# Performance work log

Measured on AMD Instinct MI355X. Metric: run time of the kernel, lower is better.

## Reference

```python
import jax, jax.numpy as jnp
import numpy as np

N, M, D, H = 100000, 1600000, 128, 1
ITERS = 10          # props
ALPHA = 0.1
GAMMA = 1.0 - ALPHA # self.gamma = ones(1,H,C)*(1-alpha)
EPS = 1e-16


def _xavier(key, fan_in, fan_out):
    bound = float(np.sqrt(6.0 / (fan_in + fan_out)))
    return jax.random.uniform(key, (fan_in, fan_out), jnp.float32, -bound, bound)


def setup_inputs() -> dict:
    key = jax.random.key(0)
    k0, k1, k2, k3 = jax.random.split(key, 4)
    x = jax.random.normal(k0, (N, D), jnp.float32)
    e = jax.random.randint(k1, (2, M), 0, N, dtype=jnp.int64)
    lin_w = _xavier(k2, D, D)          # self.lin_w
    lin_b = jnp.zeros((1, H, D // H), jnp.float32)  # self.lin_b
    skip_w = _xavier(k3, D, D)         # self.skip_connections[0]
    ln_g = jnp.ones((D,), jnp.float32)  # LayerNorm weight
    ln_b = jnp.zeros((D,), jnp.float32) # LayerNorm bias
    return {"x": x, "e": e, "lin_w": lin_w, "lin_b": lin_b,
            "skip_w": skip_w, "ln_g": ln_g, "ln_b": ln_b}


def _ppr_power(e, w, x, gamma, iters):
    # PPR.ppr with power-iteration solver, tol=0, basis=None, T=False.
    n = x.shape[0]
    s = jax.lax.stop_gradient(jnp.max(jnp.abs(x)))  # x.detach().abs().max()
    xs = x / s

    def spmv(z):
        # scatter(w.unsqueeze(-1) * z[e[1]], e[0], dim=0, reduce='sum')
        src = w[..., None] * z[e[1]]                 # (m, H, C)
        return jax.ops.segment_sum(src, e[0], num_segments=n)

    def step(z, _):
        z = gamma * spmv(z) + (1.0 - gamma) * xs
        return z, None

    z, _ = jax.lax.scan(step, jnp.zeros_like(xs), None, length=iters)
    return z * s


def reference(x, e, lin_w, lin_b, skip_w, ln_g, ln_b):
    n, m = x.shape[0], e.shape[1]
    C = D // H
    v = (x @ lin_w).reshape(n, H, C)

    # weighted=False branch: w = zeros(m, H) -> attention logits are 0,
    # softmax over each source node's out-edges gives w_ij = 1/deg(i).
    deg = jax.ops.segment_sum(jnp.ones((m, H), x.dtype), e[0], num_segments=n)
    w = 1.0 / (deg + EPS)[e[0]]                      # (m, H)

    z = _ppr_power(e, w, v, GAMMA, ITERS)            # (n, H, C)

    # skip connection + bias + post LayerNorm
    z = z + (x @ skip_w).reshape(n, H, C)
    z = (z + lin_b).reshape(n, D)
    mu = jnp.mean(z, axis=-1, keepdims=True)
    var = jnp.mean((z - mu) ** 2, axis=-1, keepdims=True)
    out = (z - mu) * jax.lax.rsqrt(var + 1e-5) * ln_g + ln_b
    return out
```

## Files before the change

### kernel.cpp

```cpp
#include <hip/hip_runtime.h>
#include <hip/hip_bf16.h>

#define N_NODES 100000
#define M_EDGES 1600000
#define DIM 128

#define BUCKET_SHIFT 9
#define BUCKET_NODES 512
#define NB 196
#define CAP 10240
#define PA_BLOCKS 512
#define PA_CHUNK (M_EDGES / PA_BLOCKS)

typedef unsigned int uint32;
typedef unsigned short ushort;
typedef __attribute__((ext_vector_type(8))) short short8;
typedef __attribute__((ext_vector_type(4))) float f32x4;
typedef __attribute__((ext_vector_type(2))) float f32x2;

__device__ __forceinline__ uint32 pack_bf16_pair(float a, float b) {
    uint32 ua = __float_as_uint(a);
    uint32 ub = __float_as_uint(b);
    ua += 0x7fffu + ((ua >> 16) & 1u);
    ub += 0x7fffu + ((ub >> 16) & 1u);
    return (ua >> 16) | (ub & 0xffff0000u);
}
__device__ __forceinline__ ushort bf16_1(float f) {
    uint32 u = __float_as_uint(f);
    u += 0x7fffu + ((u >> 16) & 1u);
    return (ushort)(u >> 16);
}
__device__ __forceinline__ float2 unpack_bf16_pair(uint32 u) {
    float2 r;
    r.x = __uint_as_float(u << 16);
    r.y = __uint_as_float(u & 0xffff0000u);
    return r;
}

__device__ __forceinline__ uint32 pack2_fp8(float a, float b) {
    return (uint32)__builtin_amdgcn_cvt_pk_fp8_f32(a, b, 0, false);
}
__device__ __forceinline__ f32x2 unpack2_fp8(uint32 u) {
    return __builtin_amdgcn_cvt_pk_f32_fp8((int)u, false);
}

__global__ __launch_bounds__(256) void partA(const int* __restrict__ e0,
                                             const int* __restrict__ e1,
                                             int* __restrict__ g_cnt,
                                             uint32* __restrict__ pairs) {
    __shared__ int hist[NB];
    __shared__ int base[NB];
    const int tid = threadIdx.x;
    const int beg = blockIdx.x * PA_CHUNK;
    const int end = beg + PA_CHUNK;
    for (int i = tid; i < NB; i += 256) hist[i] = 0;
    __syncthreads();
    #pragma unroll 4
    for (int i = beg + tid; i < end; i += 256)
        atomicAdd(&hist[e0[i] >> BUCKET_SHIFT], 1);
    __syncthreads();
    for (int i = tid; i < NB; i += 256) {
        base[i] = atomicAdd(&g_cnt[i], hist[i]);
        hist[i] = 0;
    }
    __syncthreads();
    #pragma unroll 4
    for (int i = beg + tid; i < end; i += 256) {
        const int d = e0[i];
        const int s = e1[i];
        const int b = d >> BUCKET_SHIFT;
        const int off = atomicAdd(&hist[b], 1);
        pairs[b * CAP + base[b] + off] =
            ((uint32)s << BUCKET_SHIFT) | (uint32)(d & (BUCKET_NODES - 1));
    }
}

__global__ __launch_bounds__(256) void bucket_scan(const int* __restrict__ g_cnt,
                                                   int* __restrict__ g_base,
                                                   int* __restrict__ row_ptr) {
    __shared__ int woff[4];
    const int tid  = threadIdx.x;
    const int lane = tid & 63;
    const int wid  = tid >> 6;
    const int val  = (tid < NB) ? g_cnt[tid] : 0;
    int incl = val;
    #pragma unroll
    for (int o = 1; o < 64; o <<= 1) {
        int t = __shfl_up(incl, o, 64);
        if (lane >= o) incl += t;
    }
    if (lane == 63) woff[wid] = incl;
    __syncthreads();
    if (tid == 0) {
        int a = woff[0], b = woff[1], c = woff[2];
        woff[0] = 0; woff[1] = a; woff[2] = a + b; woff[3] = a + b + c;
    }
    __syncthreads();
    if (tid < NB) g_base[tid] = woff[wid] + incl - val;
    if (tid == 0) row_ptr[N_NODES] = M_EDGES;
}

__global__ __launch_bounds__(256) void partB(const int* __restrict__ g_cnt,
                                             const int* __restrict__ g_base,
                                             const uint32* __restrict__ pairs,
                                             int* __restrict__ row_ptr,
                                             int* __restrict__ csr) {
    __shared__ int deg[BUCKET_NODES];
    __shared__ int off[BUCKET_NODES];
    __shared__ int woff[4];
    const int b     = blockIdx.x;
    const int cnt   = g_cnt[b];
    const int gbase = g_base[b];
    const int n0    = b << BUCKET_SHIFT;
    const int tid   = threadIdx.x;
    deg[tid] = 0;
    deg[tid + 256] = 0;
    __syncthreads();
    #pragma unroll 4
    for (int j = tid; j < cnt; j += 256)
        atomicAdd(&deg[pairs[b * CAP + j] & (BUCKET_NODES - 1)], 1);
    __syncthreads();
    const int lane = tid & 63;
    const int wid  = tid >> 6;
    const int d0 = deg[2 * tid];
    const int d1 = deg[2 * tid + 1];
    const int sum = d0 + d1;
    int incl = sum;
    #pragma unroll
    for (int o = 1; o < 64; o <<= 1) {
        int t = __shfl_up(incl, o, 64);
        if (lane >= o) incl += t;
    }
    if (lane == 63) woff[wid] = incl;
    __syncthreads();
    if (tid == 0) {
        int a = woff[0], bb = woff[1], c = woff[2];
        woff[0] = 0; woff[1] = a; woff[2] = a + bb; woff[3] = a + bb + c;
    }
    __syncthreads();
    const int excl = woff[wid] + incl - sum;
    off[2 * tid]     = excl;
    off[2 * tid + 1] = excl + d0;
    const int node0 = n0 + 2 * tid;
    if (node0 < N_NODES)     row_ptr[node0]     = gbase + excl;
    if (node0 + 1 < N_NODES) row_ptr[node0 + 1] = gbase + excl + d0;
    __syncthreads();
    #pragma unroll 4
    for (int j = tid; j < cnt; j += 256) {
        const uint32 code = pairs[b * CAP + j];
        const int l = code & (BUCKET_NODES - 1);
        const int p = atomicAdd(&off[l], 1);
        csr[gbase + p] = (int)(code >> BUCKET_SHIFT);
    }
}

__global__ __launch_bounds__(256) void convert_x(const float* __restrict__ x,
                                                 uint32* __restrict__ xb) {
    const int i = blockIdx.x * 256 + threadIdx.x;
    const float4 a = ((const float4*)x)[2 * i];
    const float4 b = ((const float4*)x)[2 * i + 1];
    uint4 o;
    o.x = pack_bf16_pair(a.x, a.y);
    o.y = pack_bf16_pair(a.z, a.w);
    o.z = pack_bf16_pair(b.x, b.y);
    o.w = pack_bf16_pair(b.z, b.w);
    ((uint4*)xb)[i] = o;
}

__global__ __launch_bounds__(256) void convert_w(const float* __restrict__ lin_w,
                                                 const float* __restrict__ skip_w,
                                                 ushort* __restrict__ wt) {
    const int t = blockIdx.x * 256 + threadIdx.x;
    const int c = t >> 7;
    const int k = t & 127;
    const float val = (c < DIM) ? lin_w[k * DIM + c] : skip_w[k * DIM + (c - DIM)];
    wt[t] = bf16_1(val);
}

__global__ __launch_bounds__(256) void gemm_mfma(const ushort* __restrict__ xb,
                                                 const ushort* __restrict__ wt,
                                                 ushort* __restrict__ vb,
                                                 ushort* __restrict__ skipb) {
    __shared__ short8 As[64 * 16];
    __shared__ short8 Bs[256 * 16];
    const int tid  = threadIdx.x;
    const int row0 = blockIdx.x * 64;

    #pragma unroll
    for (int it = 0; it < 4; ++it) {
        const int idx = it * 256 + tid;
        const int r = idx >> 4, c = idx & 15;
        short8 val = (short8)0;
        if (row0 + r < N_NODES)
            val = *(const short8*)&xb[(size_t)(row0 + r) * DIM + c * 8];
        As[r * 16 + (c ^ (r & 7))] = val;
    }
    #pragma unroll
    for (int it = 0; it < 16; ++it) {
        const int idx = it * 256 + tid;
        const int r = idx >> 4, c = idx & 15;
        Bs[r * 16 + (c ^ (r & 7))] = *(const short8*)&wt[(size_t)r * DIM + c * 8];
    }
    __syncthreads();

    const int lane = tid & 63;
    const int wid  = tid >> 6;
    const int n0   = wid * 64;
    const int lrow = lane & 15;
    const int lgrp = lane >> 4;

    f32x4 acc[4][4];
    #pragma unroll
    for (int m = 0; m < 4; ++m)
        #pragma unroll
        for (int n = 0; n < 4; ++n) acc[m][n] = (f32x4)0.f;

    #pragma unroll
    for (int kk = 0; kk < 4; ++kk) {
        const int ch = kk * 4 + lgrp;
        short8 a[4], b[4];
        #pragma unroll
        for (int m = 0; m < 4; ++m) {
            const int r = m * 16 + lrow;
            a[m] = As[r * 16 + (ch ^ (r & 7))];
        }
        #pragma unroll
        for (int n = 0; n < 4; ++n) {
            const int r = n0 + n * 16 + lrow;
            b[n] = Bs[r * 16 + (ch ^ (r & 7))];
        }
        #pragma unroll
        for (int m = 0; m < 4; ++m)
            #pragma unroll
            for (int n = 0; n < 4; ++n)
                acc[m][n] = __builtin_amdgcn_mfma_f32_16x16x32_bf16(a[m], b[n], acc[m][n], 0, 0, 0);
    }

    ushort* dst = (wid < 2) ? vb : skipb;
    const int cbase = (wid < 2) ? n0 : n0 - 128;
    #pragma unroll
    for (int m = 0; m < 4; ++m) {
        #pragma unroll
        for (int n = 0; n < 4; ++n) {
            #pragma unroll
            for (int r = 0; r < 4; ++r) {
                const int row = row0 + m * 16 + lgrp * 4 + r;
                if (row < N_NODES)
                    dst[(size_t)row * DIM + cbase + n * 16 + lrow] = bf16_1(acc[m][n][r]);
            }
        }
    }
}

__global__ __launch_bounds__(256) void ppr_init_fp8(const uint32* __restrict__ vb,
                                                    uint32* __restrict__ z) {
    const int i = blockIdx.x * 256 + threadIdx.x;
    const float2 a = unpack_bf16_pair(vb[2 * i]);
    const float2 b = unpack_bf16_pair(vb[2 * i + 1]);
    int p = __builtin_amdgcn_cvt_pk_fp8_f32(0.1f * a.x, 0.1f * a.y, 0, false);
    p = __builtin_amdgcn_cvt_pk_fp8_f32(0.1f * b.x, 0.1f * b.y, p, true);
    z[i] = (uint32)p;
}

__global__ __launch_bounds__(256) void spmv_fp8(const int* __restrict__ row_ptr,
                                                const int* __restrict__ csr,
                                                const ushort* __restrict__ zin,
                                                const uint32* __restrict__ vb,
                                                ushort* __restrict__ zout) {
    const int node = blockIdx.x * 4 + (threadIdx.x >> 6);
    if (node >= N_NODES) return;
    const int lane  = threadIdx.x & 63;
    const int start = row_ptr[node];
    const int end   = row_ptr[node + 1];
    float ax0 = 0.f, ay0 = 0.f, ax1 = 0.f, ay1 = 0.f;
    float ax2 = 0.f, ay2 = 0.f, ax3 = 0.f, ay3 = 0.f;
    int j = start;
    for (; j + 4 <= end; j += 4) {
        const int s0 = csr[j], s1 = csr[j + 1], s2 = csr[j + 2], s3 = csr[j + 3];
        const f32x2 t0 = unpack2_fp8(zin[(size_t)s0 * 64 + lane]);
        const f32x2 t1 = unpack2_fp8(zin[(size_t)s1 * 64 + lane]);
        const f32x2 t2 = unpack2_fp8(zin[(size_t)s2 * 64 + lane]);
        const f32x2 t3 = unpack2_fp8(zin[(size_t)s3 * 64 + lane]);
        ax0 += t0.x; ay0 += t0.y;
        ax1 += t1.x; ay1 += t1.y;
        ax2 += t2.x; ay2 += t2.y;
        ax3 += t3.x; ay3 += t3.y;
    }
    for (; j < end; ++j) {
        const f32x2 t0 = unpack2_fp8(zin[(size_t)csr[j] * 64 + lane]);
        ax0 += t0.x; ay0 += t0.y;
    }
    const float invd = 1.0f / ((float)(end - start) + 1e-16f);
    const float2 vv = unpack_bf16_pair(vb[(size_t)node * 64 + lane]);
    const float ox = 0.9f * ((ax0 + ax1) + (ax2 + ax3)) * invd + 0.1f * vv.x;
    const float oy = 0.9f * ((ay0 + ay1) + (ay2 + ay3)) * invd + 0.1f * vv.y;
    zout[(size_t)node * 64 + lane] = (ushort)pack2_fp8(ox, oy);
}

__global__ __launch_bounds__(256) void spmv_final_ln(const int* __restrict__ row_ptr,
                                                     const int* __restrict__ csr,
                                                     const ushort* __restrict__ zin,
                                                     const uint32* __restrict__ vb,
                                                     const uint32* __restrict__ skipb,
                                                     const float* __restrict__ lin_b,
                                                     const float* __restrict__ ln_g,
                                                     const float* __restrict__ ln_b,
                                                     float* __restrict__ out) {
    const int node = blockIdx.x * 4 + (threadIdx.x >> 6);
    if (node >= N_NODES) return;
    const int lane  = threadIdx.x & 63;
    const int start = row_ptr[node];
    const int end   = row_ptr[node + 1];
    float ax0 = 0.f, ay0 = 0.f, ax1 = 0.f, ay1 = 0.f;
    float ax2 = 0.f, ay2 = 0.f, ax3 = 0.f, ay3 = 0.f;
    int j = start;
    for (; j + 4 <= end; j += 4) {
        const int s0 = csr[j], s1 = csr[j + 1], s2 = csr[j + 2], s3 = csr[j + 3];
        const f32x2 t0 = unpack2_fp8(zin[(size_t)s0 * 64 + lane]);
        const f32x2 t1 = unpack2_fp8(zin[(size_t)s1 * 64 + lane]);
        const f32x2 t2 = unpack2_fp8(zin[(size_t)s2 * 64 + lane]);
        const f32x2 t3 = unpack2_fp8(zin[(size_t)s3 * 64 + lane]);
        ax0 += t0.x; ay0 += t0.y;
        ax1 += t1.x; ay1 += t1.y;
        ax2 += t2.x; ay2 += t2.y;
        ax3 += t3.x; ay3 += t3.y;
    }
    for (; j < end; ++j) {
        const f32x2 t0 = unpack2_fp8(zin[(size_t)csr[j] * 64 + lane]);
        ax0 += t0.x; ay0 += t0.y;
    }
    const float invd = 1.0f / ((float)(end - start) + 1e-16f);
    const float2 vv = unpack_bf16_pair(vb[(size_t)node * 64 + lane]);
    const float2 sk = unpack_bf16_pair(skipb[(size_t)node * 64 + lane]);
    const float2 lb = *(const float2*)&lin_b[lane * 2];
    float tx = 0.9f * ((ax0 + ax1) + (ax2 + ax3)) * invd + 0.1f * vv.x + sk.x + lb.x;
    float ty = 0.9f * ((ay0 + ay1) + (ay2 + ay3)) * invd + 0.1f * vv.y + sk.y + lb.y;

    float s = tx + ty;
    float q = tx * tx + ty * ty;
    #pragma unroll
    for (int off = 32; off; off >>= 1) {
        s += __shfl_xor(s, off, 64);
        q += __shfl_xor(q, off, 64);
    }
    const float mu   = s * (1.0f / 128.0f);
    const float var  = q * (1.0f / 128.0f) - mu * mu;
    const float rstd = rsqrtf(var + 1e-5f);
    const float2 g = *(const float2*)&ln_g[lane * 2];
    const float2 b = *(const float2*)&ln_b[lane * 2];
    float2 o;
    o.x = (tx - mu) * rstd * g.x + b.x;
    o.y = (ty - mu) * rstd * g.y + b.y;
    *(float2*)&out[(size_t)node * DIM + lane * 2] = o;
}

extern "C" void kernel_launch(void* const* d_in, const int* in_sizes, int n_in,
                              void* d_out, int out_size, void* d_ws, size_t ws_size,
                              hipStream_t stream) {
    const float* x      = (const float*)d_in[0];
    const int*   e      = (const int*)d_in[1];
    const float* lin_w  = (const float*)d_in[2];
    const float* lin_b  = (const float*)d_in[3];
    const float* skip_w = (const float*)d_in[4];
    const float* ln_g   = (const float*)d_in[5];
    const float* ln_b   = (const float*)d_in[6];
    float* out = (float*)d_out;

    const int* e0 = e;
    const int* e1 = e + M_EDGES;

    char* ws = (char*)d_ws;
    const size_t hsz = (size_t)N_NODES * DIM * sizeof(ushort);
    const size_t qsz = (size_t)N_NODES * DIM;
    const size_t psz = (size_t)NB * CAP * sizeof(uint32);
    ushort* vb    = (ushort*)(ws);
    ushort* skipb = (ushort*)(ws + hsz);
    ushort* xb    = (ushort*)(ws + 2 * hsz);
    ushort* zA    = (ushort*)(ws + 3 * hsz);
    ushort* zB    = (ushort*)(ws + 3 * hsz + qsz);
    ushort* wt    = (ushort*)(ws + 3 * hsz + 2 * qsz);
    uint32* pairs = (uint32*)(ws + 3 * hsz + 2 * qsz + 65536);
    int* row_ptr  = (int*)(ws + 3 * hsz + 2 * qsz + 65536 + psz);
    int* g_cnt    = row_ptr + (N_NODES + 1);
    int* g_base   = g_cnt + NB;
    int* csr      = g_base + NB + 2;

    hipMemsetAsync(g_cnt, 0, NB * sizeof(int), stream);
    partA<<<PA_BLOCKS, 256, 0, stream>>>(e0, e1, g_cnt, pairs);
    bucket_scan<<<1, 256, 0, stream>>>(g_cnt, g_base, row_ptr);
    partB<<<NB, 256, 0, stream>>>(g_cnt, g_base, pairs, row_ptr, csr);

    convert_x<<<(N_NODES * DIM / 8) / 256, 256, 0, stream>>>(x, (uint32*)xb);
    convert_w<<<(2 * DIM * DIM) / 256, 256, 0, stream>>>(lin_w, skip_w, wt);
    gemm_mfma<<<(N_NODES + 63) / 64, 256, 0, stream>>>(xb, wt, vb, skipb);

    ppr_init_fp8<<<(N_NODES * DIM / 4) / 256, 256, 0, stream>>>((const uint32*)vb, (uint32*)zA);
    for (int it = 0; it < 8; ++it) {
        const ushort* zi = (it & 1) ? zB : zA;
        ushort*       zo = (it & 1) ? zA : zB;
        spmv_fp8<<<N_NODES / 4, 256, 0, stream>>>(row_ptr, csr, zi, (const uint32*)vb, zo);
    }
    spmv_final_ln<<<N_NODES / 4, 256, 0, stream>>>(row_ptr, csr, zA, (const uint32*)vb,
                                                   (const uint32*)skipb, lin_b, ln_g, ln_b, out);
}
```

Baseline: 802.2 us.

## Process two nodes per wavefront in SpMV and fuse x conversion into GEMM

SpMV kernels now assign a half-wavefront (32 lanes) per node, with each lane loading 4 fp8 values as one 32-bit word. This doubles nodes per block and halves the gather instructions per edge, improving memory-level parallelism for low-degree rows. The two halves loop up to the larger degree, with masked tail iterations, so imbalance between the paired nodes wastes some lanes. Separately, the fp32-to-bf16 conversion of x is folded into the GEMM tile load, removing the convert_x kernel and the bf16 copy of x in workspace.

```diff
diff --git a/kernel.cpp b/kernel.cpp
--- a/kernel.cpp
+++ b/kernel.cpp
@@ -37,11 +37,15 @@
     return r;
 }
 
-__device__ __forceinline__ uint32 pack2_fp8(float a, float b) {
-    return (uint32)__builtin_amdgcn_cvt_pk_fp8_f32(a, b, 0, false);
-}
-__device__ __forceinline__ f32x2 unpack2_fp8(uint32 u) {
-    return __builtin_amdgcn_cvt_pk_f32_fp8((int)u, false);
+__device__ __forceinline__ uint32 pack4_fp8(float a, float b, float c, float d) {
+    int p = __builtin_amdgcn_cvt_pk_fp8_f32(a, b, 0, false);
+    p = __builtin_amdgcn_cvt_pk_fp8_f32(c, d, p, true);
+    return (uint32)p;
+}
+__device__ __forceinline__ float4 unpack4_fp8(uint32 u) {
+    const f32x2 lo = __builtin_amdgcn_cvt_pk_f32_fp8((int)u, false);
+    const f32x2 hi = __builtin_amdgcn_cvt_pk_f32_fp8((int)u, true);
+    return make_float4(lo.x, lo.y, hi.x, hi.y);
 }
 
 __global__ __launch_bounds__(256) void partA(const int* __restrict__ e0,
@@ -154,19 +158,6 @@
     }
 }
 
-__global__ __launch_bounds__(256) void convert_x(const float* __restrict__ x,
-                                                 uint32* __restrict__ xb) {
-    const int i = blockIdx.x * 256 + threadIdx.x;
-    const float4 a = ((const float4*)x)[2 * i];
-    const float4 b = ((const float4*)x)[2 * i + 1];
-    uint4 o;
-    o.x = pack_bf16_pair(a.x, a.y);
-    o.y = pack_bf16_pair(a.z, a.w);
-    o.z = pack_bf16_pair(b.x, b.y);
-    o.w = pack_bf16_pair(b.z, b.w);
-    ((uint4*)xb)[i] = o;
-}
-
 __global__ __launch_bounds__(256) void convert_w(const float* __restrict__ lin_w,
                                                  const float* __restrict__ skip_w,
                                                  ushort* __restrict__ wt) {
@@ -177,12 +168,12 @@
     wt[t] = bf16_1(val);
 }
 
-__global__ __launch_bounds__(256) void gemm_mfma(const ushort* __restrict__ xb,
+__global__ __launch_bounds__(256) void gemm_mfma(const float* __restrict__ x,
                                                  const ushort* __restrict__ wt,
                                                  ushort* __restrict__ vb,
                                                  ushort* __restrict__ skipb) {
-    __shared__ short8 As[64 * 16];
-    __shared__ short8 Bs[256 * 16];
+    __shared__ uint4 As[64 * 16];
+    __shared__ uint4 Bs[256 * 16];
     const int tid  = threadIdx.x;
     const int row0 = blockIdx.x * 64;
 
@@ -190,16 +181,23 @@
     for (int it = 0; it < 4; ++it) {
         const int idx = it * 256 + tid;
         const int r = idx >> 4, c = idx & 15;
-        short8 val = (short8)0;
-        if (row0 + r < N_NODES)
-            val = *(const short8*)&xb[(size_t)(row0 + r) * DIM + c * 8];
-        As[r * 16 + (c ^ (r & 7))] = val;
+        const int row = row0 + r;
+        uint4 o = make_uint4(0, 0, 0, 0);
+        if (row < N_NODES) {
+            const float4 f0 = *(const float4*)&x[(size_t)row * DIM + c * 8];
+            const float4 f1 = *(const float4*)&x[(size_t)row * DIM + c * 8 + 4];
+            o.x = pack_bf16_pair(f0.x, f0.y);
+            o.y = pack_bf16_pair(f0.z, f0.w);
+            o.z = pack_bf16_pair(f1.x, f1.y);
+            o.w = pack_bf16_pair(f1.z, f1.w);
+        }
+        As[r * 16 + (c ^ (r & 7))] = o;
     }
     #pragma unroll
     for (int it = 0; it < 16; ++it) {
         const int idx = it * 256 + tid;
         const int r = idx >> 4, c = idx & 15;
-        Bs[r * 16 + (c ^ (r & 7))] = *(const short8*)&wt[(size_t)r * DIM + c * 8];
+        Bs[r * 16 + (c ^ (r & 7))] = *(const uint4*)&wt[(size_t)r * DIM + c * 8];
     }
     __syncthreads();
 
@@ -222,12 +220,12 @@
         #pragma unroll
         for (int m = 0; m < 4; ++m) {
             const int r = m * 16 + lrow;
-            a[m] = As[r * 16 + (ch ^ (r & 7))];
+            a[m] = *(const short8*)&As[r * 16 + (ch ^ (r & 7))];
         }
         #pragma unroll
         for (int n = 0; n < 4; ++n) {
             const int r = n0 + n * 16 + lrow;
-            b[n] = Bs[r * 16 + (ch ^ (r & 7))];
+            b[n] = *(const short8*)&Bs[r * 16 + (ch ^ (r & 7))];
         }
         #pragma unroll
         for (int m = 0; m < 4; ++m)
@@ -257,101 +255,139 @@
     const int i = blockIdx.x * 256 + threadIdx.x;
     const float2 a = unpack_bf16_pair(vb[2 * i]);
     const float2 b = unpack_bf16_pair(vb[2 * i + 1]);
-    int p = __builtin_amdgcn_cvt_pk_fp8_f32(0.1f * a.x, 0.1f * a.y, 0, false);
-    p = __builtin_amdgcn_cvt_pk_fp8_f32(0.1f * b.x, 0.1f * b.y, p, true);
-    z[i] = (uint32)p;
+    z[i] = pack4_fp8(0.1f * a.x, 0.1f * a.y, 0.1f * b.x, 0.1f * b.y);
 }
 
 __global__ __launch_bounds__(256) void spmv_fp8(const int* __restrict__ row_ptr,
                                                 const int* __restrict__ csr,
-                                                const ushort* __restrict__ zin,
+                                                const uint32* __restrict__ zin,
                                                 const uint32* __restrict__ vb,
-                                                ushort* __restrict__ zout) {
-    const int node = blockIdx.x * 4 + (threadIdx.x >> 6);
-    if (node >= N_NODES) return;
-    const int lane  = threadIdx.x & 63;
+                                                uint32* __restrict__ zout) {
+    const int node = blockIdx.x * 8 + (threadIdx.x >> 5);
+    const int l    = threadIdx.x & 31;
     const int start = row_ptr[node];
-    const int end   = row_ptr[node + 1];
-    float ax0 = 0.f, ay0 = 0.f, ax1 = 0.f, ay1 = 0.f;
-    float ax2 = 0.f, ay2 = 0.f, ax3 = 0.f, ay3 = 0.f;
-    int j = start;
-    for (; j + 4 <= end; j += 4) {
+    const int cnt   = row_ptr[node + 1] - start;
+    const int ocnt  = __shfl_xor(cnt, 32, 64);
+    const int mn = min(cnt, ocnt);
+    const int mx = max(cnt, ocnt);
+
+    float4 acc0 = make_float4(0.f, 0.f, 0.f, 0.f);
+    float4 acc1 = make_float4(0.f, 0.f, 0.f, 0.f);
+    int k = 0;
+    #pragma unroll 2
+    for (; k + 4 <= mn; k += 4) {
+        const int j = start + k;
         const int s0 = csr[j], s1 = csr[j + 1], s2 = csr[j + 2], s3 = csr[j + 3];
-        const f32x2 t0 = unpack2_fp8(zin[(size_t)s0 * 64 + lane]);
-        const f32x2 t1 = unpack2_fp8(zin[(size_t)s1 * 64 + lane]);
-        const f32x2 t2 = unpack2_fp8(zin[(size_t)s2 * 64 + lane]);
-        const f32x2 t3 = unpack2_fp8(zin[(size_t)s3 * 64 + lane]);
-        ax0 += t0.x; ay0 += t0.y;
-        ax1 += t1.x; ay1 += t1.y;
-        ax2 += t2.x; ay2 += t2.y;
-        ax3 += t3.x; ay3 += t3.y;
-    }
-    for (; j < end; ++j) {
-        const f32x2 t0 = unpack2_fp8(zin[(size_t)csr[j] * 64 + lane]);
-        ax0 += t0.x; ay0 += t0.y;
-    }
-    const float invd = 1.0f / ((float)(end - start) + 1e-16f);
-    const float2 vv = unpack_bf16_pair(vb[(size_t)node * 64 + lane]);
-    const float ox = 0.9f * ((ax0 + ax1) + (ax2 + ax3)) * invd + 0.1f * vv.x;
-    const float oy = 0.9f * ((ay0 + ay1) + (ay2 + ay3)) * invd + 0.1f * vv.y;
-    zout[(size_t)node * 64 + lane] = (ushort)pack2_fp8(ox, oy);
+        const uint32 w0 = zin[(s0 << 5) + l];
+        const uint32 w1 = zin[(s1 << 5) + l];
+        const uint32 w2 = zin[(s2 << 5) + l];
+        const uint32 w3 = zin[(s3 << 5) + l];
+        const float4 u0 = unpack4_fp8(w0);
+        const float4 u1 = unpack4_fp8(w1);
+        const float4 u2 = unpack4_fp8(w2);
+        const float4 u3 = unpack4_fp8(w3);
+        acc0.x += u0.x + u1.x; acc0.y += u0.y + u1.y;
+        acc0.z += u0.z + u1.z; acc0.w += u0.w + u1.w;
+        acc1.x += u2.x + u3.x; acc1.y += u2.y + u3.y;
+        acc1.z += u2.z + u3.z; acc1.w += u2.w + u3.w;
+    }
+    for (; k < mx; ++k) {
+        const bool valid = k < cnt;
+        const int j = valid ? start + k : 0;
+        const int s = csr[j];
+        const float4 u = unpack4_fp8(zin[(s << 5) + l]);
+        if (valid) {
+            acc0.x += u.x; acc0.y += u.y; acc0.z += u.z; acc0.w += u.w;
+        }
+    }
+    const float invd = 0.9f / ((float)cnt + 1e-16f);
+    const uint2 vv2 = *(const uint2*)&vb[(size_t)node * 64 + 2 * l];
+    const float2 va = unpack_bf16_pair(vv2.x);
+    const float2 vbp = unpack_bf16_pair(vv2.y);
+    const float ox = (acc0.x + acc1.x) * invd + 0.1f * va.x;
+    const float oy = (acc0.y + acc1.y) * invd + 0.1f * va.y;
+    const float oz = (acc0.z + acc1.z) * invd + 0.1f * vbp.x;
+    const float ow = (acc0.w + acc1.w) * invd + 0.1f * vbp.y;
+    zout[(node << 5) + l] = pack4_fp8(ox, oy, oz, ow);
 }
 
 __global__ __launch_bounds__(256) void spmv_final_ln(const int* __restrict__ row_ptr,
                                                      const int* __restrict__ csr,
-                                                     const ushort* __restrict__ zin,
+                                                     const uint32* __restrict__ zin,
                                                      const uint32* __restrict__ vb,
                                                      const uint32* __restrict__ skipb,
                                                      const float* __restrict__ lin_b,
                                                      const float* __restrict__ ln_g,
                                                      const float* __restrict__ ln_b,
                                                      float* __restrict__ out) {
-    const int node = blockIdx.x * 4 + (threadIdx.x >> 6);
-    if (node >= N_NODES) return;
-    const int lane  = threadIdx.x & 63;
+    const int node = blockIdx.x * 8 + (threadIdx.x >> 5);
+    const int l    = threadIdx.x & 31;
     const int start = row_ptr[node];
-    const int end   = row_ptr[node + 1];
-    float ax0 = 0.f, ay0 = 0.f, ax1 = 0.f, ay1 = 0.f;
-    float ax2 = 0.f, ay2 = 0.f, ax3 = 0.f, ay3 = 0.f;
-    int j = start;
-    for (; j + 4 <= end; j += 4) {
+    const int cnt   = row_ptr[node + 1] - start;
+    const int ocnt  = __shfl_xor(cnt, 32, 64);
+    const int mn = min(cnt, ocnt);
+    const int mx = max(cnt, ocnt);
+
+    float4 acc0 = make_float4(0.f, 0.f, 0.f, 0.f);
+    float4 acc1 = make_float4(0.f, 0.f, 0.f, 0.f);
+    int k = 0;
+    #pragma unroll 2
+    for (; k + 4 <= mn; k += 4) {
+        const int j = start + k;
         const int s0 = csr[j], s1 = csr[j + 1], s2 = csr[j + 2], s3 = csr[j + 3];
-        const f32x2 t0 = unpack2_fp8(zin[(size_t)s0 * 64 + lane]);
-        const f32x2 t1 = unpack2_fp8(zin[(size_t)s1 * 64 + lane]);
-        const f32x2 t2 = unpack2_fp8(zin[(size_t)s2 * 64 + lane]);
-        const f32x2 t3 = unpack2_fp8(zin[(size_t)s3 * 64 + lane]);
-        ax0 += t0.x; ay0 += t0.y;
-        ax1 += t1.x; ay1 += t1.y;
-        ax2 += t2.x; ay2 += t2.y;
-        ax3 += t3.x; ay3 += t3.y;
-    }
-    for (; j < end; ++j) {
-        const f32x2 t0 = unpack2_fp8(zin[(size_t)csr[j] * 64 + lane]);
-        ax0 += t0.x; ay0 += t0.y;
-    }
-    const float invd = 1.0f / ((float)(end - start) + 1e-16f);
-    const float2 vv = unpack_bf16_pair(vb[(size_t)node * 64 + lane]);
-    const float2 sk = unpack_bf16_pair(skipb[(size_t)node * 64 + lane]);
-    const float2 lb = *(const float2*)&lin_b[lane * 2];
-    float tx = 0.9f * ((ax0 + ax1) + (ax2 + ax3)) * invd + 0.1f * vv.x + sk.x + lb.x;
-    float ty = 0.9f * ((ay0 + ay1) + (ay2 + ay3)) * invd + 0.1f * vv.y + sk.y + lb.y;
-
-    float s = tx + ty;
-    float q = tx * tx + ty * ty;
-    #pragma unroll
-    for (int off = 32; off; off >>= 1) {
+        const uint32 w0 = zin[(s0 << 5) + l];
+        const uint32 w1 = zin[(s1 << 5) + l];
+        const uint32 w2 = zin[(s2 << 5) + l];
+        const uint32 w3 = zin[(s3 << 5) + l];
+        const float4 u0 = unpack4_fp8(w0);
+        const float4 u1 = unpack4_fp8(w1);
+        const float4 u2 = unpack4_fp8(w2);
+        const float4 u3 = unpack4_fp8(w3);
+        acc0.x += u0.x + u1.x; acc0.y += u0.y + u1.y;
+        acc0.z += u0.z + u1.z; acc0.w += u0.w + u1.w;
+        acc1.x += u2.x + u3.x; acc1.y += u2.y + u3.y;
+        acc1.z += u2.z + u3.z; acc1.w += u2.w + u3.w;
+    }
+    for (; k < mx; ++k) {
+        const bool valid = k < cnt;
+        const int j = valid ? start + k : 0;
+        const int s = csr[j];
+        const float4 u = unpack4_fp8(zin[(s << 5) + l]);
+        if (valid) {
+            acc0.x += u.x; acc0.y += u.y; acc0.z += u.z; acc0.w += u.w;
+        }
+    }
+    const float invd = 0.9f / ((float)cnt + 1e-16f);
+    const uint2 vv2 = *(const uint2*)&vb[(size_t)node * 64 + 2 * l];
+    const uint2 ss2 = *(const uint2*)&skipb[(size_t)node * 64 + 2 * l];
+    const float2 va = unpack_bf16_pair(vv2.x);
+    const float2 vbp = unpack_bf16_pair(vv2.y);
+    const float2 sa = unpack_bf16_pair(ss2.x);
+    const float2 sb = unpack_bf16_pair(ss2.y);
+    const float4 lb = *(const float4*)&lin_b[4 * l];
+    float tx = (acc0.x + acc1.x) * invd + 0.1f * va.x + sa.x + lb.x;
+    float ty = (acc0.y + acc1.y) * invd + 0.1f * va.y + sa.y + lb.y;
+    float tz = (acc0.z + acc1.z) * invd + 0.1f * vbp.x + sb.x + lb.z;
+    float tw = (acc0.w + acc1.w) * invd + 0.1f * vbp.y + sb.y + lb.w;
+
+    float s = tx + ty + tz + tw;
+    float q = tx * tx + ty * ty + tz * tz + tw * tw;
+    #pragma unroll
+    for (int off = 16; off; off >>= 1) {
         s += __shfl_xor(s, off, 64);
         q += __shfl_xor(q, off, 64);
     }
     const float mu   = s * (1.0f / 128.0f);
     const float var  = q * (1.0f / 128.0f) - mu * mu;
     const float rstd = rsqrtf(var + 1e-5f);
-    const float2 g = *(const float2*)&ln_g[lane * 2];
-    const float2 b = *(const float2*)&ln_b[lane * 2];
-    float2 o;
+    const float4 g = *(const float4*)&ln_g[4 * l];
+    const float4 b = *(const float4*)&ln_b[4 * l];
+    float4 o;
     o.x = (tx - mu) * rstd * g.x + b.x;
     o.y = (ty - mu) * rstd * g.y + b.y;
-    *(float2*)&out[(size_t)node * DIM + lane * 2] = o;
+    o.z = (tz - mu) * rstd * g.z + b.z;
+    o.w = (tw - mu) * rstd * g.w + b.w;
+    *(float4*)&out[(size_t)node * DIM + 4 * l] = o;
 }
 
 extern "C" void kernel_launch(void* const* d_in, const int* in_sizes, int n_in,
@@ -375,12 +411,11 @@
     const size_t psz = (size_t)NB * CAP * sizeof(uint32);
     ushort* vb    = (ushort*)(ws);
     ushort* skipb = (ushort*)(ws + hsz);
-    ushort* xb    = (ushort*)(ws + 2 * hsz);
-    ushort* zA    = (ushort*)(ws + 3 * hsz);
-    ushort* zB    = (ushort*)(ws + 3 * hsz + qsz);
-    ushort* wt    = (ushort*)(ws + 3 * hsz + 2 * qsz);
-    uint32* pairs = (uint32*)(ws + 3 * hsz + 2 * qsz + 65536);
-    int* row_ptr  = (int*)(ws + 3 * hsz + 2 * qsz + 65536 + psz);
+    ushort* zA    = (ushort*)(ws + 2 * hsz);
+    ushort* zB    = (ushort*)(ws + 2 * hsz + qsz);
+    ushort* wt    = (ushort*)(ws + 2 * hsz + 2 * qsz);
+    uint32* pairs = (uint32*)(ws + 2 * hsz + 2 * qsz + 65536);
+    int* row_ptr  = (int*)(ws + 2 * hsz + 2 * qsz + 65536 + psz);
     int* g_cnt    = row_ptr + (N_NODES + 1);
     int* g_base   = g_cnt + NB;
     int* csr      = g_base + NB + 2;
@@ -390,16 +425,17 @@
     bucket_scan<<<1, 256, 0, stream>>>(g_cnt, g_base, row_ptr);
     partB<<<NB, 256, 0, stream>>>(g_cnt, g_base, pairs, row_ptr, csr);
 
-    convert_x<<<(N_NODES * DIM / 8) / 256, 256, 0, stream>>>(x, (uint32*)xb);
     convert_w<<<(2 * DIM * DIM) / 256, 256, 0, stream>>>(lin_w, skip_w, wt);
-    gemm_mfma<<<(N_NODES + 63) / 64, 256, 0, stream>>>(xb, wt, vb, skipb);
+    gemm_mfma<<<(N_NODES + 63) / 64, 256, 0, stream>>>(x, wt, vb, skipb);
 
     ppr_init_fp8<<<(N_NODES * DIM / 4) / 256, 256, 0, stream>>>((const uint32*)vb, (uint32*)zA);
     for (int it = 0; it < 8; ++it) {
         const ushort* zi = (it & 1) ? zB : zA;
         ushort*       zo = (it & 1) ? zA : zB;
-        spmv_fp8<<<N_NODES / 4, 256, 0, stream>>>(row_ptr, csr, zi, (const uint32*)vb, zo);
-    }
-    spmv_final_ln<<<N_NODES / 4, 256, 0, stream>>>(row_ptr, csr, zA, (const uint32*)vb,
-                                                   (const uint32*)skipb, lin_b, ln_g, ln_b, out);
-}
+        spmv_fp8<<<N_NODES / 8, 256, 0, stream>>>(row_ptr, csr, (const uint32*)zi,
+                                                  (const uint32*)vb, (uint32*)zo);
+    }
+    spmv_final_ln<<<N_NODES / 8, 256, 0, stream>>>(row_ptr, csr, (const uint32*)zA,
+                                                   (const uint32*)vb, (const uint32*)skipb,
+                                                   lin_b, ln_g, ln_b, out);
+}
```

Result: faster. 703.7 us (-12.3%).
